# Kernel optimization log

Measured on AMD Instinct MI355X. Metric: run time of the kernel, lower is better.

The kernel has to match this reference:

```python
import jax, jax.numpy as jnp
import numpy as np

DIM_H = 1024
DIM_S = 1024
DIM_U = 1024
DIM_Z = 128
DT_OVER_TAU = 0.1  # dt=0.1, tau=1
GAIN = 4.0


def setup_inputs() -> dict:
    key = jax.random.key(0)
    k = jax.random.split(key, 5)
    B, T = 128, 512
    h0 = jax.random.normal(k[0], (B, DIM_H), dtype=jnp.float32)
    s_seq = jax.random.normal(k[1], (B, T, DIM_S), dtype=jnp.float32)
    u_seq = jax.random.normal(k[2], (B, T, DIM_U), dtype=jnp.float32)
    # parameters per torch init
    W = jax.random.normal(k[3], (DIM_H, DIM_H), dtype=jnp.float32) * (GAIN / np.sqrt(DIM_H))
    b = jnp.zeros((DIM_H,), dtype=jnp.float32)
    Bs = jnp.eye(DIM_H, DIM_S, dtype=jnp.float32)
    Bu = jnp.eye(DIM_H, DIM_U, dtype=jnp.float32)
    Wz = jax.random.normal(k[4], (DIM_Z, DIM_H), dtype=jnp.float32) * (1.0 / np.sqrt(DIM_Z))
    bz = jnp.zeros((DIM_Z,), dtype=jnp.float32)
    return {"h0": h0, "s_seq": s_seq, "u_seq": u_seq, "W": W, "b": b,
            "Bs": Bs, "Bu": Bu, "Wz": Wz, "bz": bz}


def reference(h0, s_seq, u_seq, W, b, Bs, Bu, Wz, bz):
    a = DT_OVER_TAU
    # Precompute input drive for all timesteps: Bs@s_t + Bu@u_t + b  -> [B,T,H]
    drive = jnp.einsum('hs,bts->bth', Bs, s_seq) + jnp.einsum('hu,btu->bth', Bu, u_seq) + b
    # Only steps t=0..T-2 are consumed to produce h_1..h_{T-1}
    drive_t = jnp.swapaxes(drive[:, :-1, :], 0, 1)  # [T-1,B,H]

    def step(h, d):
        h_next = (1.0 - a) * h + a * jnp.tanh(h @ W.T + d)
        return h_next, h_next

    _, hs = jax.lax.scan(step, h0, drive_t)          # hs: [T-1,B,H]
    h_seq = jnp.concatenate([h0[:, None, :], jnp.swapaxes(hs, 0, 1)], axis=1)  # [B,T,H]
    z_seq = jnp.einsum('zh,bth->btz', Wz, h_seq) + bz                          # [B,T,Z]
    return h_seq, z_seq
```

## Files before the change

kernel.cpp:

```cpp
#include <hip/hip_runtime.h>
#include <cstdint>
#include <cmath>

#define DIM_H 1024
#define DIM_Z 128
#define NBATCH 128
#define NT 512
#define A_DT   0.1f
#define OMA_DT 0.9f

typedef short bf16x8 __attribute__((ext_vector_type(8)));
typedef float f32x4  __attribute__((ext_vector_type(4)));
#define MFMA16 __builtin_amdgcn_mfma_f32_16x16x32_bf16

#define HX_BYTE_OFF 16384
#define HX_PLANE 262144
#define HX_PAR   131072

__device__ __forceinline__ void store_u32_dev(unsigned* p, unsigned v){
  asm volatile("global_store_dword %0, %1, off sc0 sc1" :: "v"(p), "v"(v) : "memory");
}
__device__ __forceinline__ void store_u16_dev(unsigned short* p, unsigned v){
  asm volatile("global_store_short %0, %1, off sc0 sc1" :: "v"(p), "v"(v) : "memory");
}
__device__ __forceinline__ int4 load_i4_dev(const unsigned short* p){
  int4 r;
  asm volatile("global_load_dwordx4 %0, %1, off sc0 sc1" : "=v"(r) : "v"(p) : "memory");
  return r;
}
__device__ __forceinline__ unsigned load_u32_dev(const unsigned* p){
  unsigned r;
  asm volatile("global_load_dword %0, %1, off sc0 sc1\n\ts_waitcnt vmcnt(0)"
               : "=v"(r) : "v"(p) : "memory");
  return r;
}
__device__ __forceinline__ void wait_vm0(){
  asm volatile("s_waitcnt vmcnt(0)" ::: "memory");
}
__device__ __forceinline__ unsigned cvt_pk_bf16(float a, float b){
  unsigned r;
  asm("v_cvt_pk_bf16_f32 %0, %1, %2" : "=v"(r) : "v"(a), "v"(b));
  return r;
}

__global__ void k_init(unsigned* w){
  int i = blockIdx.x*1024 + threadIdx.x;
  w[i] = (i == 0) ? 1u : 0u;
}

__global__ void k_check(const float* __restrict__ Bs, const float* __restrict__ Bu,
                        const float* __restrict__ bias, unsigned* w){
  const size_t n1 = (size_t)DIM_H * DIM_H;
  const size_t total = 2*n1 + DIM_H;
  bool bad = false;
  for (size_t e = (size_t)blockIdx.x*blockDim.x + threadIdx.x; e < total;
       e += (size_t)gridDim.x*blockDim.x){
    float v, ex;
    if (e < n1)       { v = Bs[e];      ex = ((e>>10)==(e&1023)) ? 1.f : 0.f; }
    else if (e < 2*n1){ size_t e2=e-n1; v = Bu[e2]; ex = ((e2>>10)==(e2&1023)) ? 1.f : 0.f; }
    else              { v = bias[e-2*n1]; ex = 0.f; }
    if (v != ex) bad = true;
  }
  if (bad) atomicAnd(&w[0], 0u);
}

__global__ void k_drive_general(const float* __restrict__ s_seq, const float* __restrict__ u_seq,
                                const float* __restrict__ Bs, const float* __restrict__ Bu,
                                const float* __restrict__ bias, float* __restrict__ hseq,
                                const unsigned* __restrict__ w){
  if (w[0]) return;
  __shared__ float sl[DIM_H], ul[DIM_H];
  for (int pt = blockIdx.x; pt < NBATCH*(NT-1); pt += gridDim.x){
    int b = pt/(NT-1), t = pt%(NT-1);
    const float* sp = s_seq + ((size_t)b*NT + t)*DIM_H;
    const float* up = u_seq + ((size_t)b*NT + t)*DIM_H;
    __syncthreads();
    for (int k = threadIdx.x; k < DIM_H; k += blockDim.x){ sl[k]=sp[k]; ul[k]=up[k]; }
    __syncthreads();
    for (int r = threadIdx.x; r < DIM_H; r += blockDim.x){
      float acc = bias[r];
      const float* br = Bs + (size_t)r*DIM_H;
      const float* cr = Bu + (size_t)r*DIM_H;
      for (int k=0;k<DIM_H;k++) acc = fmaf(br[k], sl[k], acc);
      for (int k=0;k<DIM_H;k++) acc = fmaf(cr[k], ul[k], acc);
      hseq[((size_t)b*NT + (t+1))*DIM_H + r] = acc;
    }
  }
}

__attribute__((amdgpu_flat_work_group_size(256,256)))
__attribute__((amdgpu_waves_per_eu(1)))
__global__ void k_rnn(const float* __restrict__ h0, const float* __restrict__ s_seq,
                      const float* __restrict__ u_seq, const float* __restrict__ W,
                      const float* __restrict__ bias, float* __restrict__ hseq,
                      unsigned* __restrict__ wsp){
  const int tid  = threadIdx.x;
  const int lane = tid & 63;
  const int kq   = tid >> 6;
  const int g    = blockIdx.x >> 5;
  const int rb   = blockIdx.x & 31;
  const int row0 = rb * 32;
  const int b0   = g * 16;
  unsigned* prog = wsp + 64 + g*64;
  const int fast = (int)wsp[0];
  unsigned short* hxb = (unsigned short*)((char*)wsp + HX_BYTE_OFF);

  __shared__ __align__(16) unsigned WL[2][2][32][256];
  __shared__ __align__(16) float LP[2][4][64][4];

  {
    const int crl = tid >> 3;
    const int rt = crl >> 4, lr = crl & 15;
    const int kbase = (tid & 7) * 128;
    const float* wr = W + (size_t)(row0 + crl)*DIM_H + kbase;
    for (int kk = 0; kk < 128; kk += 8){
      int k = kbase + kk;
      float4 x = *(const float4*)(wr + kk);
      float4 y = *(const float4*)(wr + kk + 4);
      unsigned h01 = cvt_pk_bf16(x.x, x.y), h23 = cvt_pk_bf16(x.z, x.w);
      unsigned h45 = cvt_pk_bf16(y.x, y.y), h67 = cvt_pk_bf16(y.z, y.w);
      float l0 = x.x - __uint_as_float(h01 << 16);
      float l1 = x.y - __uint_as_float(h01 & 0xffff0000u);
      float l2 = x.z - __uint_as_float(h23 << 16);
      float l3 = x.w - __uint_as_float(h23 & 0xffff0000u);
      float l4 = y.x - __uint_as_float(h45 << 16);
      float l5 = y.y - __uint_as_float(h45 & 0xffff0000u);
      float l6 = y.z - __uint_as_float(h67 << 16);
      float l7 = y.w - __uint_as_float(h67 & 0xffff0000u);
      unsigned L01 = cvt_pk_bf16(l0, l1), L23 = cvt_pk_bf16(l2, l3);
      unsigned L45 = cvt_pk_bf16(l4, l5), L67 = cvt_pk_bf16(l6, l7);
      int c = k >> 5, kg = (k & 31) >> 3, li = kg*16 + lr;
      *(uint4*)&WL[rt][0][c][li*4] = make_uint4(h01, h23, h45, h67);
      *(uint4*)&WL[rt][1][c][li*4] = make_uint4(L01, L23, L45, L67);
    }
  }

  const int rowin = tid & 15;
  const int bl    = tid >> 4;
  const int bb    = b0 + bl;
  const int r0g   = row0 + rowin;
  const int r1g   = row0 + 16 + rowin;
  const int laneC = ((rowin >> 2) << 4) | bl;
  const int regC  = rowin & 3;
  const float bias0 = bias[r0g], bias1 = bias[r1g];

  const size_t loff = (size_t)(b0 + (lane & 15))*1024 + kq*256 + (lane >> 4)*8;
  const unsigned short* pH0 = hxb + 0*HX_PLANE + 0*HX_PAR + loff;
  const unsigned short* pH1 = hxb + 0*HX_PLANE + 1*HX_PAR + loff;
  const unsigned short* pL0 = hxb + 1*HX_PLANE + 0*HX_PAR + loff;
  const unsigned short* pL1 = hxb + 1*HX_PLANE + 1*HX_PAR + loff;

  float hold0 = h0[(size_t)bb*DIM_H + r0g];
  float hold1 = h0[(size_t)bb*DIM_H + r1g];
  hseq[((size_t)bb*NT + 0)*DIM_H + r0g] = hold0;
  hseq[((size_t)bb*NT + 0)*DIM_H + r1g] = hold1;
  {
    unsigned p0 = cvt_pk_bf16(hold0, hold0);
    unsigned q0 = cvt_pk_bf16(hold0 - __uint_as_float(p0 << 16), 0.f);
    unsigned p1 = cvt_pk_bf16(hold1, hold1);
    unsigned q1 = cvt_pk_bf16(hold1 - __uint_as_float(p1 << 16), 0.f);
    store_u16_dev(hxb + 0*HX_PLANE + (size_t)bb*1024 + r0g, p0);
    store_u16_dev(hxb + 1*HX_PLANE + (size_t)bb*1024 + r0g, q0);
    store_u16_dev(hxb + 0*HX_PLANE + (size_t)bb*1024 + r1g, p1);
    store_u16_dev(hxb + 1*HX_PLANE + (size_t)bb*1024 + r1g, q1);
  }
  float sv0=0.f, uv0=0.f, sv1=0.f, uv1=0.f;
  if (fast){
    size_t o0 = ((size_t)bb*NT + 0)*DIM_H + r0g;
    size_t o1 = ((size_t)bb*NT + 0)*DIM_H + r1g;
    sv0 = s_seq[o0]; uv0 = u_seq[o0];
    sv1 = s_seq[o1]; uv1 = u_seq[o1];
  }
  wait_vm0();
  __syncthreads();
  if (tid == 0) store_u32_dev(prog + rb, 1u);

  for (int t = 0; t < NT-1; t++){
    if (tid < 64){
      const unsigned* pp = prog + (lane & 31);
      for(;;){
        unsigned v = load_u32_dev(pp);
        if (__all(v >= (unsigned)(t+1))) break;
        __builtin_amdgcn_s_sleep(1);
      }
    }
    __syncthreads();

    const unsigned short* pH = (t & 1) ? pH1 : pH0;
    const unsigned short* pL = (t & 1) ? pL1 : pL0;
    int4 sB[8][2];
    #pragma unroll
    for (int ks = 0; ks < 8; ks++){
      sB[ks][0] = load_i4_dev(pH + ks*32);
      sB[ks][1] = load_i4_dev(pL + ks*32);
    }

    float dv0, dv1;
    if (fast){
      dv0 = sv0 + uv0 + bias0;
      dv1 = sv1 + uv1 + bias1;
    } else {
      dv0 = hseq[((size_t)bb*NT + (t+1))*DIM_H + r0g];
      dv1 = hseq[((size_t)bb*NT + (t+1))*DIM_H + r1g];
    }

    wait_vm0();
    __builtin_amdgcn_sched_barrier(0);

    f32x4 c00{0,0,0,0}, c01{0,0,0,0}, c02{0,0,0,0}, c03{0,0,0,0};
    f32x4 c10{0,0,0,0}, c11{0,0,0,0}, c12{0,0,0,0}, c13{0,0,0,0};
    #pragma unroll
    for (int ks = 0; ks < 8; ks++){
      bf16x8 bh = __builtin_bit_cast(bf16x8, sB[ks][0]);
      bf16x8 bl2 = __builtin_bit_cast(bf16x8, sB[ks][1]);
      const int c = kq*8 + ks;
      bf16x8 a0h = *(const bf16x8*)&WL[0][0][c][lane*4];
      bf16x8 a0l = *(const bf16x8*)&WL[0][1][c][lane*4];
      bf16x8 a1h = *(const bf16x8*)&WL[1][0][c][lane*4];
      bf16x8 a1l = *(const bf16x8*)&WL[1][1][c][lane*4];
      c00 = MFMA16(a0h, bh,  c00, 0,0,0);
      c01 = MFMA16(a0h, bl2, c01, 0,0,0);
      c02 = MFMA16(a0l, bh,  c02, 0,0,0);
      c03 = MFMA16(a0l, bl2, c03, 0,0,0);
      c10 = MFMA16(a1h, bh,  c10, 0,0,0);
      c11 = MFMA16(a1h, bl2, c11, 0,0,0);
      c12 = MFMA16(a1l, bh,  c12, 0,0,0);
      c13 = MFMA16(a1l, bl2, c13, 0,0,0);
    }
    f32x4 C0 = (c00 + c01) + (c02 + c03);
    f32x4 C1 = (c10 + c11) + (c12 + c13);
    *(f32x4*)&LP[0][kq][lane][0] = C0;
    *(f32x4*)&LP[1][kq][lane][0] = C1;
    __syncthreads();

    float pre0 = (LP[0][0][laneC][regC] + LP[0][1][laneC][regC])
               + (LP[0][2][laneC][regC] + LP[0][3][laneC][regC]);
    float pre1 = (LP[1][0][laneC][regC] + LP[1][1][laneC][regC])
               + (LP[1][2][laneC][regC] + LP[1][3][laneC][regC]);
    float hn0 = OMA_DT*hold0 + A_DT*tanhf(pre0 + dv0);
    float hn1 = OMA_DT*hold1 + A_DT*tanhf(pre1 + dv1);
    hold0 = hn0; hold1 = hn1;
    hseq[((size_t)bb*NT + (t+1))*DIM_H + r0g] = hn0;
    hseq[((size_t)bb*NT + (t+1))*DIM_H + r1g] = hn1;
    {
      const size_t q = (size_t)((t+1) & 1) * HX_PAR;
      unsigned p0 = cvt_pk_bf16(hn0, hn0);
      unsigned q0 = cvt_pk_bf16(hn0 - __uint_as_float(p0 << 16), 0.f);
      unsigned p1 = cvt_pk_bf16(hn1, hn1);
      unsigned q1 = cvt_pk_bf16(hn1 - __uint_as_float(p1 << 16), 0.f);
      store_u16_dev(hxb + 0*HX_PLANE + q + (size_t)bb*1024 + r0g, p0);
      store_u16_dev(hxb + 1*HX_PLANE + q + (size_t)bb*1024 + r0g, q0);
      store_u16_dev(hxb + 0*HX_PLANE + q + (size_t)bb*1024 + r1g, p1);
      store_u16_dev(hxb + 1*HX_PLANE + q + (size_t)bb*1024 + r1g, q1);
    }
    if (fast){
      size_t o0 = ((size_t)bb*NT + (t+1))*DIM_H + r0g;
      size_t o1 = ((size_t)bb*NT + (t+1))*DIM_H + r1g;
      sv0 = s_seq[o0]; uv0 = u_seq[o0];
      sv1 = s_seq[o1]; uv1 = u_seq[o1];
    }
    wait_vm0();
    __syncthreads();
    if (tid == 0) store_u32_dev(prog + rb, (unsigned)(t+2));
  }
}

#define GLD_LDS16(gp, lp) \
  __builtin_amdgcn_global_load_lds((const __attribute__((address_space(1))) void*)(gp), \
                                   (__attribute__((address_space(3))) void*)(lp), 16, 0, 0)
#define DOT4(hv, wv, a) do { \
  a = fmaf((hv).x, (wv).x, a); a = fmaf((hv).y, (wv).y, a); \
  a = fmaf((hv).z, (wv).z, a); a = fmaf((hv).w, (wv).w, a); } while(0)

__device__ __forceinline__ float wave_sum64(float x){
  x += __int_as_float(__builtin_amdgcn_update_dpp(0, __float_as_int(x), 0x111, 0xf, 0xf, true));
  x += __int_as_float(__builtin_amdgcn_update_dpp(0, __float_as_int(x), 0x112, 0xf, 0xf, true));
  x += __int_as_float(__builtin_amdgcn_update_dpp(0, __float_as_int(x), 0x114, 0xf, 0xf, true));
  x += __int_as_float(__builtin_amdgcn_update_dpp(0, __float_as_int(x), 0x118, 0xf, 0xf, true));
  x += __int_as_float(__builtin_amdgcn_update_dpp(0, __float_as_int(x), 0x142, 0xf, 0xf, true));
  x += __int_as_float(__builtin_amdgcn_update_dpp(0, __float_as_int(x), 0x143, 0xf, 0xf, true));
  return x;
}

__launch_bounds__(256, 1)
__global__ void k_z(const float* __restrict__ hseq, const float* __restrict__ Wz,
                    const float* __restrict__ bz, float* __restrict__ z){
  const int tid = threadIdx.x, lane = tid & 63, wv = tid >> 6;
  const size_t pos0 = (size_t)blockIdx.x * 16;
  __shared__ __align__(16) float h_lds[16*DIM_H];
  __shared__ __align__(16) float out_lds[512];
  #pragma unroll
  for (int i=0;i<16;i++){
    const float* src = hseq + (pos0+i)*DIM_H + tid*4;
    GLD_LDS16(src, &h_lds[i*DIM_H + tid*4]);
  }
  asm volatile("s_waitcnt vmcnt(0)" ::: "memory");
  __syncthreads();
  const int ei = tid>>5, er = tid&31;
  for (int zg=0; zg<4; zg++){
    const int zr0 = zg*32;
    float4 wreg[8][4];
    const float* wr = Wz + (size_t)(zr0 + wv*8)*DIM_H + lane*4;
    #pragma unroll
    for (int rr=0;rr<8;rr++)
      #pragma unroll
      for (int c=0;c<4;c++)
        wreg[rr][c] = *(const float4*)(wr + (size_t)rr*DIM_H + c*256);
    #pragma unroll 2
    for (int i=0;i<16;i++){
      const float4* hp = (const float4*)&h_lds[i*DIM_H];
      float4 hv0 = hp[lane], hv1 = hp[lane+64], hv2 = hp[lane+128], hv3 = hp[lane+192];
      float acc[8];
      #pragma unroll
      for (int rr=0;rr<8;rr++){
        float s = 0.f;
        DOT4(hv0, wreg[rr][0], s); DOT4(hv1, wreg[rr][1], s);
        DOT4(hv2, wreg[rr][2], s); DOT4(hv3, wreg[rr][3], s);
        acc[rr] = s;
      }
      #pragma unroll
      for (int rr=0;rr<8;rr++){
        float v = wave_sum64(acc[rr]);
        if (lane==63) out_lds[wv*128 + i*8 + rr] = v;
      }
    }
    __syncthreads();
    const int zr = zr0 + er;
    float v1 = out_lds[(er>>3)*128 + ei*8     + (er&7)] + bz[zr];
    float v2 = out_lds[(er>>3)*128 + (ei+8)*8 + (er&7)] + bz[zr];
    z[(pos0+ei)*DIM_Z + zr]   = v1;
    z[(pos0+ei+8)*DIM_Z + zr] = v2;
    __syncthreads();
  }
}

extern "C" void kernel_launch(void* const* d_in, const int* in_sizes, int n_in,
                              void* d_out, int out_size, void* d_ws, size_t ws_size,
                              hipStream_t stream){
  const float* h0    = (const float*)d_in[0];
  const float* s_seq = (const float*)d_in[1];
  const float* u_seq = (const float*)d_in[2];
  const float* W     = (const float*)d_in[3];
  const float* bias  = (const float*)d_in[4];
  const float* Bs    = (const float*)d_in[5];
  const float* Bu    = (const float*)d_in[6];
  const float* Wz    = (const float*)d_in[7];
  const float* bz    = (const float*)d_in[8];
  float* hseq = (float*)d_out;
  float* z    = hseq + (size_t)NBATCH*NT*DIM_H;
  unsigned* w = (unsigned*)d_ws;

  k_init<<<4, 1024, 0, stream>>>(w);
  k_check<<<256, 256, 0, stream>>>(Bs, Bu, bias, w);
  k_drive_general<<<2048, 256, 0, stream>>>(s_seq, u_seq, Bs, Bu, bias, hseq, w);
  {
    void* args[] = {(void*)&h0, (void*)&s_seq, (void*)&u_seq, (void*)&W,
                    (void*)&bias, (void*)&hseq, (void*)&w};
    hipError_t rc = hipLaunchCooperativeKernel((const void*)k_rnn, dim3(256), dim3(256),
                                               args, 0, stream);
    if (rc != hipSuccess){
      k_rnn<<<256, 256, 0, stream>>>(h0, s_seq, u_seq, W, bias, hseq, w);
    }
  }
  k_z<<<(NBATCH*NT)/16, 256, 0, stream>>>(hseq, Wz, bz, z);
}
```

Measured before the change: 3.422 ms.

## Interleave hi/lo bf16 state, use atomic group counter barrier, prefetch drive earlier

Packs each hidden value's hi and lo bf16 halves into one 32-bit word, so every step writes one dword per element instead of two short stores. Readers de-interleave the halves with v_perm in registers. The per-block progress flags, which a whole wave polled, become a single atomic counter per batch group polled by one thread. The s/u input loads for the next step are issued alongside the state loads rather than after the output stores. Together these aim to cut the inter-block synchronisation latency and the store traffic on the serial recurrence path, at the cost of extra permute instructions and contention on the atomic counter.

```diff
diff --git a/kernel.cpp b/kernel.cpp
--- a/kernel.cpp
+++ b/kernel.cpp
@@ -14,17 +14,13 @@
 #define MFMA16 __builtin_amdgcn_mfma_f32_16x16x32_bf16
 
 #define HX_BYTE_OFF 16384
-#define HX_PLANE 262144
-#define HX_PAR   131072
+#define HX_PAR_U32  131072
 
 __device__ __forceinline__ void store_u32_dev(unsigned* p, unsigned v){
   asm volatile("global_store_dword %0, %1, off sc0 sc1" :: "v"(p), "v"(v) : "memory");
 }
-__device__ __forceinline__ void store_u16_dev(unsigned short* p, unsigned v){
-  asm volatile("global_store_short %0, %1, off sc0 sc1" :: "v"(p), "v"(v) : "memory");
-}
-__device__ __forceinline__ int4 load_i4_dev(const unsigned short* p){
-  int4 r;
+__device__ __forceinline__ uint4 load_u4_dev(const unsigned* p){
+  uint4 r;
   asm volatile("global_load_dwordx4 %0, %1, off sc0 sc1" : "=v"(r) : "v"(p) : "memory");
   return r;
 }
@@ -41,6 +37,11 @@
   unsigned r;
   asm("v_cvt_pk_bf16_f32 %0, %1, %2" : "=v"(r) : "v"(a), "v"(b));
   return r;
+}
+__device__ __forceinline__ unsigned pack_hl(float h){
+  unsigned t = cvt_pk_bf16(h, h);
+  float res = h - __uint_as_float(t << 16);
+  return cvt_pk_bf16(h, res);
 }
 
 __global__ void k_init(unsigned* w){
@@ -101,9 +102,9 @@
   const int rb   = blockIdx.x & 31;
   const int row0 = rb * 32;
   const int b0   = g * 16;
-  unsigned* prog = wsp + 64 + g*64;
+  unsigned* gcnt = wsp + 64 + g*16;
   const int fast = (int)wsp[0];
-  unsigned short* hxb = (unsigned short*)((char*)wsp + HX_BYTE_OFF);
+  unsigned* hx32 = (unsigned*)((char*)wsp + HX_BYTE_OFF);
 
   __shared__ __align__(16) unsigned WL[2][2][32][256];
   __shared__ __align__(16) float LP[2][4][64][4];
@@ -144,26 +145,16 @@
   const int regC  = rowin & 3;
   const float bias0 = bias[r0g], bias1 = bias[r1g];
 
-  const size_t loff = (size_t)(b0 + (lane & 15))*1024 + kq*256 + (lane >> 4)*8;
-  const unsigned short* pH0 = hxb + 0*HX_PLANE + 0*HX_PAR + loff;
-  const unsigned short* pH1 = hxb + 0*HX_PLANE + 1*HX_PAR + loff;
-  const unsigned short* pL0 = hxb + 1*HX_PLANE + 0*HX_PAR + loff;
-  const unsigned short* pL1 = hxb + 1*HX_PLANE + 1*HX_PAR + loff;
+  const size_t loffu = (size_t)(b0 + (lane & 15))*1024 + kq*256 + (lane >> 4)*8;
+  const unsigned* pB0 = hx32 + loffu;
+  const unsigned* pB1 = hx32 + HX_PAR_U32 + loffu;
 
   float hold0 = h0[(size_t)bb*DIM_H + r0g];
   float hold1 = h0[(size_t)bb*DIM_H + r1g];
   hseq[((size_t)bb*NT + 0)*DIM_H + r0g] = hold0;
   hseq[((size_t)bb*NT + 0)*DIM_H + r1g] = hold1;
-  {
-    unsigned p0 = cvt_pk_bf16(hold0, hold0);
-    unsigned q0 = cvt_pk_bf16(hold0 - __uint_as_float(p0 << 16), 0.f);
-    unsigned p1 = cvt_pk_bf16(hold1, hold1);
-    unsigned q1 = cvt_pk_bf16(hold1 - __uint_as_float(p1 << 16), 0.f);
-    store_u16_dev(hxb + 0*HX_PLANE + (size_t)bb*1024 + r0g, p0);
-    store_u16_dev(hxb + 1*HX_PLANE + (size_t)bb*1024 + r0g, q0);
-    store_u16_dev(hxb + 0*HX_PLANE + (size_t)bb*1024 + r1g, p1);
-    store_u16_dev(hxb + 1*HX_PLANE + (size_t)bb*1024 + r1g, q1);
-  }
+  store_u32_dev(hx32 + (size_t)bb*1024 + r0g, pack_hl(hold0));
+  store_u32_dev(hx32 + (size_t)bb*1024 + r1g, pack_hl(hold1));
   float sv0=0.f, uv0=0.f, sv1=0.f, uv1=0.f;
   if (fast){
     size_t o0 = ((size_t)bb*NT + 0)*DIM_H + r0g;
@@ -173,32 +164,32 @@
   }
   wait_vm0();
   __syncthreads();
-  if (tid == 0) store_u32_dev(prog + rb, 1u);
+  if (tid == 0)
+    __hip_atomic_fetch_add(gcnt, 1u, __ATOMIC_RELAXED, __HIP_MEMORY_SCOPE_AGENT);
 
   for (int t = 0; t < NT-1; t++){
-    if (tid < 64){
-      const unsigned* pp = prog + (lane & 31);
-      for(;;){
-        unsigned v = load_u32_dev(pp);
-        if (__all(v >= (unsigned)(t+1))) break;
-        __builtin_amdgcn_s_sleep(1);
-      }
-    }
-    __syncthreads();
-
-    const unsigned short* pH = (t & 1) ? pH1 : pH0;
-    const unsigned short* pL = (t & 1) ? pL1 : pL0;
-    int4 sB[8][2];
+    if (tid == 0){
+      const unsigned tgt = 32u*(unsigned)(t+1);
+      while (load_u32_dev(gcnt) < tgt) __builtin_amdgcn_s_sleep(1);
+    }
+    __syncthreads();
+
+    const unsigned* pB = (t & 1) ? pB1 : pB0;
+    uint4 sB[8][2];
     #pragma unroll
     for (int ks = 0; ks < 8; ks++){
-      sB[ks][0] = load_i4_dev(pH + ks*32);
-      sB[ks][1] = load_i4_dev(pL + ks*32);
+      sB[ks][0] = load_u4_dev(pB + ks*32);
+      sB[ks][1] = load_u4_dev(pB + ks*32 + 4);
     }
 
     float dv0, dv1;
     if (fast){
       dv0 = sv0 + uv0 + bias0;
       dv1 = sv1 + uv1 + bias1;
+      size_t o0 = ((size_t)bb*NT + (t+1))*DIM_H + r0g;
+      size_t o1 = ((size_t)bb*NT + (t+1))*DIM_H + r1g;
+      sv0 = s_seq[o0]; uv0 = u_seq[o0];
+      sv1 = s_seq[o1]; uv1 = u_seq[o1];
     } else {
       dv0 = hseq[((size_t)bb*NT + (t+1))*DIM_H + r0g];
       dv1 = hseq[((size_t)bb*NT + (t+1))*DIM_H + r1g];
@@ -211,8 +202,18 @@
     f32x4 c10{0,0,0,0}, c11{0,0,0,0}, c12{0,0,0,0}, c13{0,0,0,0};
     #pragma unroll
     for (int ks = 0; ks < 8; ks++){
-      bf16x8 bh = __builtin_bit_cast(bf16x8, sB[ks][0]);
-      bf16x8 bl2 = __builtin_bit_cast(bf16x8, sB[ks][1]);
+      uint4 wa = sB[ks][0], wb = sB[ks][1];
+      uint4 bhu, blu;
+      bhu.x = __builtin_amdgcn_perm(wa.y, wa.x, 0x05040100u);
+      bhu.y = __builtin_amdgcn_perm(wa.w, wa.z, 0x05040100u);
+      bhu.z = __builtin_amdgcn_perm(wb.y, wb.x, 0x05040100u);
+      bhu.w = __builtin_amdgcn_perm(wb.w, wb.z, 0x05040100u);
+      blu.x = __builtin_amdgcn_perm(wa.y, wa.x, 0x07060302u);
+      blu.y = __builtin_amdgcn_perm(wa.w, wa.z, 0x07060302u);
+      blu.z = __builtin_amdgcn_perm(wb.y, wb.x, 0x07060302u);
+      blu.w = __builtin_amdgcn_perm(wb.w, wb.z, 0x07060302u);
+      bf16x8 bh  = __builtin_bit_cast(bf16x8, bhu);
+      bf16x8 bl2 = __builtin_bit_cast(bf16x8, blu);
       const int c = kq*8 + ks;
       bf16x8 a0h = *(const bf16x8*)&WL[0][0][c][lane*4];
       bf16x8 a0l = *(const bf16x8*)&WL[0][1][c][lane*4];
@@ -243,25 +244,14 @@
     hseq[((size_t)bb*NT + (t+1))*DIM_H + r0g] = hn0;
     hseq[((size_t)bb*NT + (t+1))*DIM_H + r1g] = hn1;
     {
-      const size_t q = (size_t)((t+1) & 1) * HX_PAR;
-      unsigned p0 = cvt_pk_bf16(hn0, hn0);
-      unsigned q0 = cvt_pk_bf16(hn0 - __uint_as_float(p0 << 16), 0.f);
-      unsigned p1 = cvt_pk_bf16(hn1, hn1);
-      unsigned q1 = cvt_pk_bf16(hn1 - __uint_as_float(p1 << 16), 0.f);
-      store_u16_dev(hxb + 0*HX_PLANE + q + (size_t)bb*1024 + r0g, p0);
-      store_u16_dev(hxb + 1*HX_PLANE + q + (size_t)bb*1024 + r0g, q0);
-      store_u16_dev(hxb + 0*HX_PLANE + q + (size_t)bb*1024 + r1g, p1);
-      store_u16_dev(hxb + 1*HX_PLANE + q + (size_t)bb*1024 + r1g, q1);
-    }
-    if (fast){
-      size_t o0 = ((size_t)bb*NT + (t+1))*DIM_H + r0g;
-      size_t o1 = ((size_t)bb*NT + (t+1))*DIM_H + r1g;
-      sv0 = s_seq[o0]; uv0 = u_seq[o0];
-      sv1 = s_seq[o1]; uv1 = u_seq[o1];
+      unsigned* hq = hx32 + (((t+1) & 1) ? HX_PAR_U32 : 0) + (size_t)bb*1024;
+      store_u32_dev(hq + r0g, pack_hl(hn0));
+      store_u32_dev(hq + r1g, pack_hl(hn1));
     }
     wait_vm0();
     __syncthreads();
-    if (tid == 0) store_u32_dev(prog + rb, (unsigned)(t+2));
+    if (tid == 0)
+      __hip_atomic_fetch_add(gcnt, 1u, __ATOMIC_RELAXED, __HIP_MEMORY_SCOPE_AGENT);
   }
 }
 
```

Result: slower. 4.086 ms (+19.4%).
